# Kernel optimization log

Measured on AMD Instinct MI355X. Metric: run time of the kernel, lower is better.

The kernel has to match this reference:

```python
import jax, jax.numpy as jnp
import numpy as np
from jax import lax

B_, N_, DIM, HID, DST, NT, IR, DTR, HH, WW = 16, 4096, 192, 384, 16, 17, 128, 24, 64, 64


def _selective_scan(u, delta, A, Bs, Cs, D, delta_bias):
    # u, delta: (B, Din, L); A: (Din, N); Bs, Cs: (B, N, L); D, delta_bias: (Din,)
    delta = jax.nn.softplus(delta + delta_bias[None, :, None])
    dT = jnp.moveaxis(delta, 2, 0)   # (L, B, Din)
    uT = jnp.moveaxis(u, 2, 0)       # (L, B, Din)
    BT = jnp.moveaxis(Bs, 2, 0)      # (L, B, N)
    CT = jnp.moveaxis(Cs, 2, 0)      # (L, B, N)
    Bsz, Din, L = u.shape
    Nst = A.shape[1]
    h0 = jnp.zeros((Bsz, Din, Nst), u.dtype)

    def step(h, inp):
        d_l, u_l, b_l, c_l = inp
        da = jnp.exp(d_l[:, :, None] * A[None])              # (B, Din, N)
        h = da * h + (d_l * u_l)[:, :, None] * b_l[:, None, :]
        y = jnp.einsum('bdn,bn->bd', h, c_l)
        return h, y

    _, ys = lax.scan(step, h0, (dT, uT, BT, CT))
    y = jnp.moveaxis(ys, 0, 2)                               # (B, Din, L)
    return y + u * D[None, :, None]


def _assm_forward(x, token_weight, gumbel_noise, embB, route_w1, route_b1, route_w2,
                  route_b2, inproj_w, inproj_b, cpe_w, cpe_b, x_proj_w, dt_w, dt_b,
                  A_logs, Ds, norm_g, norm_b, outproj_w, outproj_b, H, W, gather_type):
    B, n, C = x.shape
    hidden = inproj_w.shape[0]
    dst = token_weight.shape[1]
    dtr = dt_w.shape[1]

    # routing + gumbel-softmax (hard, straight-through)
    full_emb = embB @ token_weight                           # (NT, d_state)
    hmid = jax.nn.gelu(x @ route_w1.T + route_b1)
    logits = jax.nn.log_softmax(hmid @ route_w2.T + route_b2, axis=-1)
    y_soft = jax.nn.softmax(logits + gumbel_noise, axis=-1)
    idx = jnp.argmax(y_soft, axis=-1)                        # (B, n)
    y_hard = jax.nn.one_hot(idx, logits.shape[-1], dtype=y_soft.dtype)
    cls_policy = y_hard + y_soft - lax.stop_gradient(y_soft)
    prompt = cls_policy @ full_emb                           # (B, n, d_state)

    det = lax.stop_gradient(idx)
    # (gather_type 3/5 keypoint-group remap omitted: gather_type == 1 here)
    sort_idx = jnp.argsort(det, axis=-1)                     # (B, n)
    inv_idx = jnp.argsort(sort_idx, axis=-1)                 # index_reverse

    # in_proj (1x1 conv == pointwise linear) then depthwise CPE gate
    xi = x @ inproj_w.T + inproj_b                           # (B, n, hidden)
    xg = xi.reshape(B, H, W, hidden).transpose(0, 3, 1, 2)   # NCHW
    cpe = lax.conv_general_dilated(xg, cpe_w, (1, 1), 'SAME',
                                   feature_group_count=hidden,
                                   dimension_numbers=('NCHW', 'OIHW', 'NCHW'))
    cpe = cpe + cpe_b[None, :, None, None]
    xg = xg * jax.nn.sigmoid(cpe)
    xflat = xg.reshape(B, hidden, n).transpose(0, 2, 1)      # (B, n, hidden)

    sem_x = jnp.take_along_axis(xflat, sort_idx[:, :, None], axis=1)

    # Selective_Scan core
    xs = sem_x.transpose(0, 2, 1)                            # (B, Din, L)
    x_dbl = jnp.einsum('bdl,cd->bcl', xs, x_proj_w)          # (B, dtr+2N, L)
    dts, Bs, Cs = jnp.split(x_dbl, [dtr, dtr + dst], axis=1)
    dts = jnp.einsum('brl,dr->bdl', dts, dt_w)
    if gather_type != 0:
        Cs = Cs + prompt.transpose(0, 2, 1)
    A = -jnp.exp(A_logs)
    y = _selective_scan(xs, dts, A, Bs, Cs, Ds, dt_b)        # (B, Din, L)
    y = y.transpose(0, 2, 1)                                 # (B, L, hidden)

    mu = jnp.mean(y, axis=-1, keepdims=True)
    var = jnp.mean(jnp.square(y - mu), axis=-1, keepdims=True)
    yn = (y - mu) / jnp.sqrt(var + 1e-5) * norm_g + norm_b
    out = yn @ outproj_w.T + outproj_b                       # (B, n, dim)
    out = jnp.take_along_axis(out, inv_idx[:, :, None], axis=1)
    return out


def setup_inputs() -> dict:
    key = jax.random.key(0)
    ks = jax.random.split(key, 16)

    def rn(k, sh, s=0.02):
        return jax.random.normal(k, sh, dtype=jnp.float32) * s

    u = jax.random.uniform(ks[0], (B_, N_, NT), jnp.float32, 1e-6, 1.0 - 1e-6)
    gumbel = -jnp.log(-jnp.log(u))

    # faithful dt bias init (inverse-softplus of log-uniform dt)
    rng = np.random.default_rng(0)
    dt = np.exp(rng.uniform(size=HID) * (np.log(0.1) - np.log(0.001)) + np.log(0.001))
    dt = np.clip(dt, 1e-4, None)
    inv_dt = dt + np.log(-np.expm1(-dt))

    A_logs = jnp.log(jnp.tile(jnp.arange(1, DST + 1, dtype=jnp.float32), (HID, 1)))

    return {
        'x': jax.random.normal(ks[1], (B_, N_, DIM), jnp.float32),
        'token_weight': rn(ks[2], (IR, DST), 0.1),
        'gumbel_noise': gumbel,
        'embB': jax.random.uniform(ks[3], (NT, IR), jnp.float32, -1.0 / NT, 1.0 / NT),
        'route_w1': rn(ks[4], (DIM // 3, DIM)),
        'route_b1': jnp.zeros((DIM // 3,), jnp.float32),
        'route_w2': rn(ks[5], (NT, DIM // 3)),
        'route_b2': jnp.zeros((NT,), jnp.float32),
        'inproj_w': rn(ks[6], (HID, DIM)),
        'inproj_b': jnp.zeros((HID,), jnp.float32),
        'cpe_w': rn(ks[7], (HID, 1, 3, 3), 0.1),
        'cpe_b': jnp.zeros((HID,), jnp.float32),
        'x_proj_w': rn(ks[8], (DTR + 2 * DST, HID)),
        'dt_w': jax.random.uniform(ks[9], (HID, DTR), jnp.float32, -DTR ** -0.5, DTR ** -0.5),
        'dt_b': jnp.asarray(inv_dt, jnp.float32),
        'A_logs': A_logs,
        'Ds': jnp.ones((HID,), jnp.float32),
        'norm_g': jnp.ones((HID,), jnp.float32),
        'norm_b': jnp.zeros((HID,), jnp.float32),
        'outproj_w': rn(ks[10], (DIM, HID)),
        'outproj_b': jnp.zeros((DIM,), jnp.float32),
        'H': HH,
        'W': WW,
        'gather_type': 1,
    }


def reference(x, token_weight, gumbel_noise, embB, route_w1, route_b1, route_w2,
              route_b2, inproj_w, inproj_b, cpe_w, cpe_b, x_proj_w, dt_w, dt_b,
              A_logs, Ds, norm_g, norm_b, outproj_w, outproj_b, H, W, gather_type):
    return _assm_forward(x, token_weight, gumbel_noise, embB, route_w1, route_b1,
                         route_w2, route_b2, inproj_w, inproj_b, cpe_w, cpe_b,
                         x_proj_w, dt_w, dt_b, A_logs, Ds, norm_g, norm_b,
                         outproj_w, outproj_b, H, W, gather_type)
```

## Files before the change

### kernel.cpp

```cpp
#include <hip/hip_runtime.h>
#include <math.h>

#define NB 16
#define NL 4096
#define ND 192
#define NH 384
#define NS 16
#define NTK 17
#define NIR 128
#define NR 24
#define NHH 64
#define NWW 64
#define NCHUNKS 32
#define CHUNKLEN 128
#define NTOK (NB*NL)

typedef __attribute__((ext_vector_type(8))) short short8;
typedef __attribute__((ext_vector_type(4))) float floatx4;

__device__ __forceinline__ float gelu_tanh(float x){
  return 0.5f*x*(1.0f + tanhf(0.7978845608028654f*(x + 0.044715f*x*x*x)));
}
__device__ __forceinline__ float softplus_f(float x){
  return (x > 20.0f) ? x : log1pf(expf(x));
}
__device__ __forceinline__ short f2bf(float f){
  unsigned u = __float_as_uint(f);
  unsigned r = (u + 0x7fffu + ((u >> 16) & 1u)) >> 16;
  return (short)r;
}

union Pack8 { uint4 v; short s[8]; };

__global__ void k_cvtw(const float* __restrict__ inw, const float* __restrict__ ow,
                       const float* __restrict__ xpw, const float* __restrict__ dtw,
                       short* __restrict__ inwb, short* __restrict__ owb,
                       short* __restrict__ xpwb, short* __restrict__ dtwb,
                       const float* __restrict__ embB, const float* __restrict__ tw,
                       float* __restrict__ fe){
  int i = blockIdx.x*256 + threadIdx.x;
  int stride = gridDim.x*256;
  for (int p = i; p < NH*ND; p += stride) inwb[p] = f2bf(inw[p]);
  for (int p = i; p < ND*NH; p += stride) owb[p] = f2bf(ow[p]);
  for (int p = i; p < 56*NH; p += stride) xpwb[p] = f2bf(xpw[p]);
  for (int p = i; p < NH*32; p += stride){
    int r = p >> 5, c = p & 31;
    dtwb[p] = (c < NR) ? f2bf(dtw[r*NR + c]) : (short)0;
  }
  if (blockIdx.x == 0){
    for (int o = threadIdx.x; o < NTK*NS; o += 256){
      int t = o / NS, s = o % NS;
      float acc = 0.f;
      for (int k = 0; k < NIR; ++k) acc += embB[t*NIR+k]*tw[k*NS+s];
      fe[o] = acc;
    }
  }
}

template<int EPI>
__global__ __launch_bounds__(256) void k_gemm(const float* __restrict__ A, int lda,
    const float* __restrict__ W, int ldw, const float* __restrict__ bias,
    float* __restrict__ C, int ldc, int N, int K){
  __shared__ float As[16][68];
  __shared__ float Ws[16][68];
  int tid = threadIdx.x;
  int m0 = blockIdx.x*64, n0 = blockIdx.y*64;
  int tx = tid & 15, ty = tid >> 4;
  int srow = tid >> 2, skseg = (tid & 3)*4;
  float acc[4][4] = {};
  for (int k0 = 0; k0 < K; k0 += 16){
    {
      const float* ap = A + (size_t)(m0+srow)*lda + k0 + skseg;
      float4 v = *(const float4*)ap;
      As[skseg+0][srow]=v.x; As[skseg+1][srow]=v.y;
      As[skseg+2][srow]=v.z; As[skseg+3][srow]=v.w;
    }
    {
      float4 v = {0.f,0.f,0.f,0.f};
      if (n0 + srow < N) v = *(const float4*)(W + (size_t)(n0+srow)*ldw + k0 + skseg);
      Ws[skseg+0][srow]=v.x; Ws[skseg+1][srow]=v.y;
      Ws[skseg+2][srow]=v.z; Ws[skseg+3][srow]=v.w;
    }
    __syncthreads();
    #pragma unroll
    for (int kk = 0; kk < 16; ++kk){
      float4 av = *(const float4*)&As[kk][ty*4];
      float4 wv = *(const float4*)&Ws[kk][tx*4];
      acc[0][0] += av.x*wv.x; acc[0][1] += av.x*wv.y;
      acc[0][2] += av.x*wv.z; acc[0][3] += av.x*wv.w;
      acc[1][0] += av.y*wv.x; acc[1][1] += av.y*wv.y;
      acc[1][2] += av.y*wv.z; acc[1][3] += av.y*wv.w;
      acc[2][0] += av.z*wv.x; acc[2][1] += av.z*wv.y;
      acc[2][2] += av.z*wv.z; acc[2][3] += av.z*wv.w;
      acc[3][0] += av.w*wv.x; acc[3][1] += av.w*wv.y;
      acc[3][2] += av.w*wv.z; acc[3][3] += av.w*wv.w;
    }
    __syncthreads();
  }
  #pragma unroll
  for (int i = 0; i < 4; ++i){
    int m = m0 + ty*4 + i;
    #pragma unroll
    for (int j = 0; j < 4; ++j){
      int n = n0 + tx*4 + j;
      if (n < N){
        float v = acc[i][j] + (bias ? bias[n] : 0.f);
        if (EPI==1) v = gelu_tanh(v);
        C[(size_t)m*ldc + n] = v;
      }
    }
  }
}

template<int EPI, int AF32, int LNA>
__global__ __launch_bounds__(256) void k_mfma(const void* __restrict__ Aptr, int lda,
    const short* __restrict__ Wbf, int ldw, const float* __restrict__ bias,
    float* __restrict__ C, int ldc, int N, int K, const int* __restrict__ remap,
    const float* __restrict__ lnm, const float* __restrict__ lnr,
    const float* __restrict__ lng, const float* __restrict__ lnb){
  __shared__ short As[128*40];
  __shared__ short Bs[64*40];
  int tid = threadIdx.x;
  int m0 = blockIdx.x*128, n0 = blockIdx.y*64;
  int w = tid >> 6, lane = tid & 63;
  int lq = lane >> 4, lr = lane & 15;
  floatx4 acc[2][4];
  #pragma unroll
  for (int i = 0; i < 2; ++i)
    #pragma unroll
    for (int j = 0; j < 4; ++j) acc[i][j] = (floatx4){0.f,0.f,0.f,0.f};
  int ar = tid >> 1, aq = (tid & 1)*2;
  int br = tid >> 2, bq = tid & 3;
  float mr = 0.f, rr = 0.f;
  if (LNA){ mr = lnm[m0+ar]; rr = lnr[m0+ar]; }
  for (int k0 = 0; k0 < K; k0 += 32){
    Pack8 sa0, sa1;
    if (AF32){
      const float* ap = (const float*)Aptr + (size_t)(m0+ar)*lda + k0 + aq*8;
      float f[16];
      float4 f0 = *(const float4*)(ap);
      float4 f1 = *(const float4*)(ap+4);
      float4 f2 = *(const float4*)(ap+8);
      float4 f3 = *(const float4*)(ap+12);
      f[0]=f0.x; f[1]=f0.y; f[2]=f0.z; f[3]=f0.w;
      f[4]=f1.x; f[5]=f1.y; f[6]=f1.z; f[7]=f1.w;
      f[8]=f2.x; f[9]=f2.y; f[10]=f2.z; f[11]=f2.w;
      f[12]=f3.x; f[13]=f3.y; f[14]=f3.z; f[15]=f3.w;
      if (LNA){
        const float* gp = lng + k0 + aq*8;
        const float* bp = lnb + k0 + aq*8;
        #pragma unroll
        for (int j = 0; j < 16; ++j) f[j] = (f[j]-mr)*rr*gp[j] + bp[j];
      }
      #pragma unroll
      for (int j = 0; j < 8; ++j){ sa0.s[j] = f2bf(f[j]); sa1.s[j] = f2bf(f[8+j]); }
    } else {
      const short* ap = (const short*)Aptr + (size_t)(m0+ar)*lda + k0 + aq*8;
      sa0.v = *(const uint4*)ap;
      sa1.v = *(const uint4*)(ap + 8);
    }
    uint4 bv = {0u,0u,0u,0u};
    if (n0 + br < N) bv = *(const uint4*)(Wbf + (size_t)(n0+br)*ldw + k0 + bq*8);
    __syncthreads();
    *(uint4*)&As[ar*40 + aq*8]     = sa0.v;
    *(uint4*)&As[ar*40 + aq*8 + 8] = sa1.v;
    *(uint4*)&Bs[br*40 + bq*8]     = bv;
    __syncthreads();
    short8 a0 = *(const short8*)&As[(w*32      + lr)*40 + lq*8];
    short8 a1 = *(const short8*)&As[(w*32 + 16 + lr)*40 + lq*8];
    short8 b0 = *(const short8*)&Bs[(     lr)*40 + lq*8];
    short8 b1 = *(const short8*)&Bs[(16 + lr)*40 + lq*8];
    short8 b2 = *(const short8*)&Bs[(32 + lr)*40 + lq*8];
    short8 b3 = *(const short8*)&Bs[(48 + lr)*40 + lq*8];
    acc[0][0] = __builtin_amdgcn_mfma_f32_16x16x32_bf16(a0, b0, acc[0][0], 0,0,0);
    acc[0][1] = __builtin_amdgcn_mfma_f32_16x16x32_bf16(a0, b1, acc[0][1], 0,0,0);
    acc[0][2] = __builtin_amdgcn_mfma_f32_16x16x32_bf16(a0, b2, acc[0][2], 0,0,0);
    acc[0][3] = __builtin_amdgcn_mfma_f32_16x16x32_bf16(a0, b3, acc[0][3], 0,0,0);
    acc[1][0] = __builtin_amdgcn_mfma_f32_16x16x32_bf16(a1, b0, acc[1][0], 0,0,0);
    acc[1][1] = __builtin_amdgcn_mfma_f32_16x16x32_bf16(a1, b1, acc[1][1], 0,0,0);
    acc[1][2] = __builtin_amdgcn_mfma_f32_16x16x32_bf16(a1, b2, acc[1][2], 0,0,0);
    acc[1][3] = __builtin_amdgcn_mfma_f32_16x16x32_bf16(a1, b3, acc[1][3], 0,0,0);
  }
  #pragma unroll
  for (int mt = 0; mt < 2; ++mt){
    #pragma unroll
    for (int r = 0; r < 4; ++r){
      int m = m0 + w*32 + mt*16 + lq*4 + r;
      int orow = (EPI==3) ? remap[m] : m;
      #pragma unroll
      for (int nt = 0; nt < 4; ++nt){
        int n = n0 + nt*16 + lr;
        if (n < N){
          float v = acc[mt][nt][r] + (bias ? bias[n] : 0.f);
          if (EPI==2) v = softplus_f(v);
          C[(size_t)orow*ldc + n] = v;
        }
      }
    }
  }
}

__global__ __launch_bounds__(256) void k_xdbl(const float* __restrict__ us,
    const short* __restrict__ xpwb, const int* __restrict__ idx,
    const float* __restrict__ fe, const int* __restrict__ gt,
    float* __restrict__ Bsb, float* __restrict__ Csb, short* __restrict__ dtsb){
  __shared__ short As[128*40];
  __shared__ short Bs[64*40];
  int tid = threadIdx.x;
  int m0 = blockIdx.x*128;
  int w = tid >> 6, lane = tid & 63;
  int lq = lane >> 4, lr = lane & 15;
  floatx4 acc[2][4];
  #pragma unroll
  for (int i = 0; i < 2; ++i)
    #pragma unroll
    for (int j = 0; j < 4; ++j) acc[i][j] = (floatx4){0.f,0.f,0.f,0.f};
  int ar = tid >> 1, aq = (tid & 1)*2;
  int br = tid >> 2, bq = tid & 3;
  for (int k0 = 0; k0 < NH; k0 += 32){
    Pack8 sa0, sa1;
    {
      const float* ap = us + (size_t)(m0+ar)*NH + k0 + aq*8;
      float f[16];
      float4 f0 = *(const float4*)(ap);
      float4 f1 = *(const float4*)(ap+4);
      float4 f2 = *(const float4*)(ap+8);
      float4 f3 = *(const float4*)(ap+12);
      f[0]=f0.x; f[1]=f0.y; f[2]=f0.z; f[3]=f0.w;
      f[4]=f1.x; f[5]=f1.y; f[6]=f1.z; f[7]=f1.w;
      f[8]=f2.x; f[9]=f2.y; f[10]=f2.z; f[11]=f2.w;
      f[12]=f3.x; f[13]=f3.y; f[14]=f3.z; f[15]=f3.w;
      #pragma unroll
      for (int j = 0; j < 8; ++j){ sa0.s[j] = f2bf(f[j]); sa1.s[j] = f2bf(f[8+j]); }
    }
    uint4 bv = {0u,0u,0u,0u};
    if (br < 56) bv = *(const uint4*)(xpwb + (size_t)br*NH + k0 + bq*8);
    __syncthreads();
    *(uint4*)&As[ar*40 + aq*8]     = sa0.v;
    *(uint4*)&As[ar*40 + aq*8 + 8] = sa1.v;
    *(uint4*)&Bs[br*40 + bq*8]     = bv;
    __syncthreads();
    short8 a0 = *(const short8*)&As[(w*32      + lr)*40 + lq*8];
    short8 a1 = *(const short8*)&As[(w*32 + 16 + lr)*40 + lq*8];
    short8 b0 = *(const short8*)&Bs[(     lr)*40 + lq*8];
    short8 b1 = *(const short8*)&Bs[(16 + lr)*40 + lq*8];
    short8 b2 = *(const short8*)&Bs[(32 + lr)*40 + lq*8];
    short8 b3 = *(const short8*)&Bs[(48 + lr)*40 + lq*8];
    acc[0][0] = __builtin_amdgcn_mfma_f32_16x16x32_bf16(a0, b0, acc[0][0], 0,0,0);
    acc[0][1] = __builtin_amdgcn_mfma_f32_16x16x32_bf16(a0, b1, acc[0][1], 0,0,0);
    acc[0][2] = __builtin_amdgcn_mfma_f32_16x16x32_bf16(a0, b2, acc[0][2], 0,0,0);
    acc[0][3] = __builtin_amdgcn_mfma_f32_16x16x32_bf16(a0, b3, acc[0][3], 0,0,0);
    acc[1][0] = __builtin_amdgcn_mfma_f32_16x16x32_bf16(a1, b0, acc[1][0], 0,0,0);
    acc[1][1] = __builtin_amdgcn_mfma_f32_16x16x32_bf16(a1, b1, acc[1][1], 0,0,0);
    acc[1][2] = __builtin_amdgcn_mfma_f32_16x16x32_bf16(a1, b2, acc[1][2], 0,0,0);
    acc[1][3] = __builtin_amdgcn_mfma_f32_16x16x32_bf16(a1, b3, acc[1][3], 0,0,0);
  }
  int gather = gt[0];
  #pragma unroll
  for (int mt = 0; mt < 2; ++mt){
    #pragma unroll
    for (int r = 0; r < 4; ++r){
      int m = m0 + w*32 + mt*16 + lq*4 + r;
      int id = idx[m];
      #pragma unroll
      for (int nt = 0; nt < 4; ++nt){
        int n = nt*16 + lr;
        float v = acc[mt][nt][r];
        if (n < 24){
          dtsb[(size_t)m*32 + n] = f2bf(v);
        } else if (n < 40){
          Bsb[(size_t)m*NS + (n-24)] = v;
          if (n < 32) dtsb[(size_t)m*32 + n] = 0;
        } else if (n < 56){
          float cv = v;
          if (gather != 0) cv += fe[id*NS + (n-40)];
          Csb[(size_t)m*NS + (n-40)] = cv;
        }
      }
    }
  }
}

__global__ __launch_bounds__(256) void k_argmax(const float* __restrict__ hmid,
    const float* __restrict__ w2, const float* __restrict__ b2,
    const float* __restrict__ gumbel, int* __restrict__ idx){
  int g = blockIdx.x*256 + threadIdx.x;
  float hm[64];
  const float4* hp = (const float4*)(hmid + (size_t)g*64);
  #pragma unroll
  for (int i = 0; i < 16; ++i){
    float4 v = hp[i];
    hm[i*4+0]=v.x; hm[i*4+1]=v.y; hm[i*4+2]=v.z; hm[i*4+3]=v.w;
  }
  float best = -INFINITY; int bi = 0;
  for (int c = 0; c < NTK; ++c){
    float s = b2[c] + gumbel[(size_t)g*NTK + c];
    #pragma unroll
    for (int j = 0; j < 64; ++j) s += hm[j]*w2[c*64+j];
    if (s > best){ best = s; bi = c; }
  }
  idx[g] = bi;
}

__global__ __launch_bounds__(256) void k_sort(const int* __restrict__ idx,
    int* __restrict__ rmap, int* __restrict__ inv){
  int b = blockIdx.x, t = threadIdx.x;
  __shared__ int hist[NTK][256];
  __shared__ int tot[NTK];
  __shared__ int keybase[NTK];
  int keys[16];
  const int* ip = idx + b*NL + t*16;
  #pragma unroll
  for (int i = 0; i < 16; ++i) keys[i] = ip[i];
  #pragma unroll
  for (int k = 0; k < NTK; ++k){
    int c = 0;
    #pragma unroll
    for (int i = 0; i < 16; ++i) c += (keys[i]==k) ? 1 : 0;
    hist[k][t] = c;
  }
  __syncthreads();
  if (t < NTK){
    int run = 0;
    for (int j = 0; j < 256; ++j){ int v = hist[t][j]; hist[t][j] = run; run += v; }
    tot[t] = run;
  }
  __syncthreads();
  if (t == 0){
    int base = 0;
    for (int k = 0; k < NTK; ++k){ keybase[k] = base; base += tot[k]; }
  }
  __syncthreads();
  #pragma unroll
  for (int i = 0; i < 16; ++i){
    int k = keys[i];
    int cb = 0;
    #pragma unroll
    for (int j = 0; j < 16; ++j) cb += (j < i && keys[j]==k) ? 1 : 0;
    int pos = keybase[k] + hist[k][t] + cb;
    rmap[b*NL + pos] = b*NL + t*16 + i;
    inv[b*NL + t*16 + i] = pos;
  }
}

__global__ __launch_bounds__(384) void k_cpe(const float* __restrict__ xi,
    const float* __restrict__ cw, const float* __restrict__ cb,
    const int* __restrict__ inv, float* __restrict__ us){
  int bl = blockIdx.x;
  int cg = bl & 3;
  int xt = (bl>>2) & 7;
  int yt = (bl>>5) & 7;
  int b  = bl >> 8;
  __shared__ float tile[10*10*96];
  int tx = threadIdx.x;
  int ty = threadIdx.y;
  int c0 = cg*96;
  int ch = c0 + tx;
  for (int yy = 0; yy < 10; ++yy){
    int gy = yt*8 + yy - 1;
    for (int xx = ty; xx < 10; xx += 4){
      int gx = xt*8 + xx - 1;
      float v = 0.f;
      if (gy >= 0 && gy < NHH && gx >= 0 && gx < NWW)
        v = xi[((size_t)(b*NL + gy*NWW + gx))*NH + ch];
      tile[(yy*10 + xx)*96 + tx] = v;
    }
  }
  float wreg[9];
  #pragma unroll
  for (int j = 0; j < 9; ++j) wreg[j] = cw[ch*9 + j];
  float bias = cb[ch];
  __syncthreads();
  for (int yy = ty; yy < 8; yy += 4){
    #pragma unroll
    for (int xx = 0; xx < 8; ++xx){
      float acc = bias;
      #pragma unroll
      for (int dy = 0; dy < 3; ++dy)
        #pragma unroll
        for (int dx = 0; dx < 3; ++dx)
          acc += tile[((yy+dy)*10 + (xx+dx))*96 + tx] * wreg[dy*3+dx];
      float center = tile[((yy+1)*10 + (xx+1))*96 + tx];
      float gate = 1.f/(1.f + expf(-acc));
      int l = (yt*8+yy)*NWW + xt*8+xx;
      int pos = inv[b*NL + l];
      us[((size_t)(b*NL + pos))*NH + ch] = center*gate;
    }
  }
}

__device__ __forceinline__ void decay16(bool pw, float dlt, const float* An, float* a){
  if (pw){
    float r  = __expf(dlt*An[0]);
    float r2 = r*r;
    float r3 = r2*r;
    float r4 = r2*r2;
    float r8 = r4*r4;
    float r12 = r8*r4;
    a[0]=r;     a[1]=r2;     a[2]=r3;     a[3]=r4;
    a[4]=r4*r;  a[5]=r4*r2;  a[6]=r4*r3;  a[7]=r8;
    a[8]=r8*r;  a[9]=r8*r2;  a[10]=r8*r3; a[11]=r12;
    a[12]=r12*r; a[13]=r12*r2; a[14]=r12*r3; a[15]=r8*r8;
  } else {
    #pragma unroll
    for (int n = 0; n < NS; ++n) a[n] = __expf(dlt*An[n]);
  }
}
__device__ __forceinline__ bool pwcheck(const float* An){
  bool pw = true;
  #pragma unroll
  for (int n = 1; n < NS; ++n)
    pw = pw && (fabsf(An[n] - (n+1)*An[0]) <= 1e-4f*fabsf(An[n]));
  return pw;
}

__global__ __launch_bounds__(384) void k_scan1(const float* __restrict__ delta,
    const float* __restrict__ us, const float* __restrict__ Bsb,
    const float* __restrict__ A_logs, float* __restrict__ sds, float* __restrict__ Boff){
  int bc = blockIdx.x;
  int c = bc & (NCHUNKS-1);
  int b = bc >> 5;
  int d = threadIdx.x;
  __shared__ float4 Bsh[CHUNKLEN*4];
  int base = b*NL + c*CHUNKLEN;
  {
    const float4* Bg = (const float4*)(Bsb + (size_t)base*NS);
    for (int p = d; p < CHUNKLEN*4; p += 384) Bsh[p] = Bg[p];
  }
  float An[NS];
  #pragma unroll
  for (int n = 0; n < NS; ++n) An[n] = -expf(A_logs[d*NS + n]);
  bool pw = pwcheck(An);
  float h[NS];
  #pragma unroll
  for (int n = 0; n < NS; ++n) h[n]=0.f;
  float sd = 0.f;
  __syncthreads();
  size_t gi = (size_t)base*NH + d;
  float dlt = delta[gi];
  float uv  = us[gi];
  #pragma unroll 2
  for (int s = 0; s < CHUNKLEN; ++s){
    float dltc = dlt, uvc = uv;
    if (s < CHUNKLEN-1){
      dlt = delta[gi + NH];
      uv  = us[gi + NH];
    }
    float du = dltc*uvc;
    sd += dltc;
    float a[NS];
    decay16(pw, dltc, An, a);
    float bb[NS];
    #pragma unroll
    for (int q = 0; q < 4; ++q) *(float4*)&bb[4*q] = Bsh[s*4 + q];
    #pragma unroll
    for (int n = 0; n < NS; ++n) h[n] = a[n]*h[n] + du*bb[n];
    gi += NH;
  }
  sds[(size_t)bc*NH + d] = sd;
  size_t o = ((size_t)bc*NH + d)*NS;
  *(float4*)(Boff + o)      = make_float4(h[0], h[1], h[2], h[3]);
  *(float4*)(Boff + o + 4)  = make_float4(h[4], h[5], h[6], h[7]);
  *(float4*)(Boff + o + 8)  = make_float4(h[8], h[9], h[10],h[11]);
  *(float4*)(Boff + o + 12) = make_float4(h[12],h[13],h[14],h[15]);
}

__global__ __launch_bounds__(256) void k_scan2(const float* __restrict__ A_logs,
    const float* __restrict__ sds, float* __restrict__ Boff){
  int i = blockIdx.x*256 + threadIdx.x;
  int dn = i % (NH*NS);
  int b = i / (NH*NS);
  float An = -expf(A_logs[dn]);
  int d = dn >> 4;
  float h = 0.f;
  for (int c = 0; c < NCHUNKS; ++c){
    int bc = b*NCHUNKS + c;
    float sd = sds[(size_t)bc*NH + d];
    float a = __expf(sd*An);
    size_t o = (size_t)bc*(NH*NS) + dn;
    float bo = Boff[o];
    Boff[o] = h;
    h = a*h + bo;
  }
}

__global__ __launch_bounds__(384) void k_scan3(const float* __restrict__ delta,
    const float* __restrict__ Bsb, const float* __restrict__ Csb,
    const float* __restrict__ A_logs, const float* __restrict__ Ds,
    const float* __restrict__ hinit, float* __restrict__ us,
    float* __restrict__ lnmean, float* __restrict__ lnrstd){
  int bc = blockIdx.x;
  int c = bc & (NCHUNKS-1);
  int b = bc >> 5;
  int d = threadIdx.x;
  __shared__ float4 Bsh[CHUNKLEN*4];
  __shared__ float4 Csh[CHUNKLEN*4];
  int base = b*NL + c*CHUNKLEN;
  {
    const float4* Bg = (const float4*)(Bsb + (size_t)base*NS);
    const float4* Cg = (const float4*)(Csb + (size_t)base*NS);
    for (int p = d; p < CHUNKLEN*4; p += 384){
      Bsh[p] = Bg[p];
      Csh[p] = Cg[p];
    }
  }
  float An[NS];
  #pragma unroll
  for (int n = 0; n < NS; ++n) An[n] = -expf(A_logs[d*NS + n]);
  bool pw = pwcheck(An);
  float h[NS];
  size_t ho = ((size_t)bc*NH + d)*NS;
  {
    float4 h0 = *(const float4*)(hinit + ho);
    float4 h1 = *(const float4*)(hinit + ho + 4);
    float4 h2 = *(const float4*)(hinit + ho + 8);
    float4 h3 = *(const float4*)(hinit + ho + 12);
    h[0]=h0.x; h[1]=h0.y; h[2]=h0.z; h[3]=h0.w;
    h[4]=h1.x; h[5]=h1.y; h[6]=h1.z; h[7]=h1.w;
    h[8]=h2.x; h[9]=h2.y; h[10]=h2.z; h[11]=h2.w;
    h[12]=h3.x; h[13]=h3.y; h[14]=h3.z; h[15]=h3.w;
  }
  float Dd = Ds[d];
  __syncthreads();
  size_t gi = (size_t)base*NH + d;
  float dlt = delta[gi];
  float uv  = us[gi];
  #pragma unroll 2
  for (int s = 0; s < CHUNKLEN; ++s){
    float dltc = dlt, uvc = uv;
    if (s < CHUNKLEN-1){
      dlt = delta[gi + NH];
      uv  = us[gi + NH];
    }
    float du = dltc*uvc;
    float a[NS];
    decay16(pw, dltc, An, a);
    float bb[NS], cc[NS];
    #pragma unroll
    for (int q = 0; q < 4; ++q){
      *(float4*)&bb[4*q] = Bsh[s*4 + q];
      *(float4*)&cc[4*q] = Csh[s*4 + q];
    }
    #pragma unroll
    for (int n = 0; n < NS; ++n) h[n] = a[n]*h[n] + du*bb[n];
    float ya = 0.f, yb = 0.f, yc = 0.f, yd = 0.f;
    #pragma unroll
    for (int q = 0; q < 4; ++q){
      ya += h[q]*cc[q];
      yb += h[4+q]*cc[4+q];
      yc += h[8+q]*cc[8+q];
      yd += h[12+q]*cc[12+q];
    }
    float y = (ya+yb)+(yc+yd);
    us[gi] = y + uvc*Dd;
    gi += NH;
  }
  __syncthreads();
  {
    int w = d >> 6, lane = d & 63;
    for (int t = w; t < CHUNKLEN; t += 6){
      int row = base + t;
      const float* rp = us + (size_t)row*NH;
      float v[6];
      #pragma unroll
      for (int i = 0; i < 6; ++i) v[i] = rp[i*64 + lane];
      float s = 0.f;
      #pragma unroll
      for (int i = 0; i < 6; ++i) s += v[i];
      #pragma unroll
      for (int off = 32; off > 0; off >>= 1) s += __shfl_xor(s, off);
      float mu = s * (1.f/NH);
      float vs = 0.f;
      #pragma unroll
      for (int i = 0; i < 6; ++i){ float dv = v[i]-mu; vs += dv*dv; }
      #pragma unroll
      for (int off = 32; off > 0; off >>= 1) vs += __shfl_xor(vs, off);
      float rs = rsqrtf(vs*(1.f/NH) + 1e-5f);
      if (lane == 0){ lnmean[row] = mu; lnrstd[row] = rs; }
    }
  }
}

extern "C" void kernel_launch(void* const* d_in, const int* in_sizes, int n_in,
                              void* d_out, int out_size, void* d_ws, size_t ws_size,
                              hipStream_t stream){
  const float* x      = (const float*)d_in[0];
  const float* tw     = (const float*)d_in[1];
  const float* gumbel = (const float*)d_in[2];
  const float* embB   = (const float*)d_in[3];
  const float* rw1    = (const float*)d_in[4];
  const float* rb1    = (const float*)d_in[5];
  const float* rw2    = (const float*)d_in[6];
  const float* rb2    = (const float*)d_in[7];
  const float* inw    = (const float*)d_in[8];
  const float* inb    = (const float*)d_in[9];
  const float* cw     = (const float*)d_in[10];
  const float* cb     = (const float*)d_in[11];
  const float* xpw    = (const float*)d_in[12];
  const float* dtw    = (const float*)d_in[13];
  const float* dtb    = (const float*)d_in[14];
  const float* A_logs = (const float*)d_in[15];
  const float* Ds     = (const float*)d_in[16];
  const float* ng     = (const float*)d_in[17];
  const float* nbv    = (const float*)d_in[18];
  const float* ow     = (const float*)d_in[19];
  const float* ob     = (const float*)d_in[20];
  const int*   gt     = (const int*)d_in[23];
  float* out = (float*)d_out;

  float* ws = (float*)d_ws;
  size_t o = 0;
  float* fe   = ws + o; o += 512;
  int* idx    = (int*)(ws + o); o += NTOK;
  int* rmap   = (int*)(ws + o); o += NTOK;
  int* inv    = (int*)(ws + o); o += NTOK;
  float* hmid = ws + o; o += (size_t)NTOK*64;
  float* xi   = ws + o; o += (size_t)NTOK*NH;
  float* us   = ws + o; o += (size_t)NTOK*NH;
  float* Bsb  = ws + o; o += (size_t)NTOK*NS;
  float* Csb  = ws + o; o += (size_t)NTOK*NS;
  float* sds  = ws + o; o += (size_t)NB*NCHUNKS*NH;
  float* Bof  = ws + o; o += (size_t)NB*NCHUNKS*NH*NS;
  short* inwb = (short*)(ws + o); o += (NH*ND)/2;
  short* owb  = (short*)(ws + o); o += (ND*NH)/2;
  short* xpwb = (short*)(ws + o); o += (56*NH)/2 + 32;
  short* dtwb = (short*)(ws + o); o += (NH*32)/2;
  float* delta = xi;
  short* dtsb = (short*)Bof;
  float* lnmean = (float*)idx;
  float* lnrstd = (float*)inv;

  k_cvtw<<<64,256,0,stream>>>(inw, ow, xpw, dtw, inwb, owb, xpwb, dtwb, embB, tw, fe);
  k_gemm<1><<<dim3(NTOK/64,1),256,0,stream>>>(x, ND, rw1, ND, rb1, hmid, 64, 64, ND);
  k_argmax<<<NTOK/256,256,0,stream>>>(hmid, rw2, rb2, gumbel, idx);
  k_sort<<<NB,256,0,stream>>>(idx, rmap, inv);
  k_mfma<0,1,0><<<dim3(NTOK/128,6),256,0,stream>>>(x, ND, inwb, ND, inb, xi, NH, NH, ND,
      nullptr, nullptr, nullptr, nullptr, nullptr);
  k_cpe<<<NB*64*4,dim3(96,4),0,stream>>>(xi, cw, cb, inv, us);
  k_xdbl<<<NTOK/128,256,0,stream>>>(us, xpwb, idx, fe, gt, Bsb, Csb, dtsb);
  k_mfma<2,0,0><<<dim3(NTOK/128,6),256,0,stream>>>(dtsb, 32, dtwb, 32, dtb, delta, NH, NH, 32,
      nullptr, nullptr, nullptr, nullptr, nullptr);
  k_scan1<<<NB*NCHUNKS,384,0,stream>>>(delta, us, Bsb, A_logs, sds, Bof);
  k_scan2<<<(NB*NH*NS)/256,256,0,stream>>>(A_logs, sds, Bof);
  k_scan3<<<NB*NCHUNKS,384,0,stream>>>(delta, Bsb, Csb, A_logs, Ds, Bof, us,
                                       lnmean, lnrstd);
  k_mfma<3,1,1><<<dim3(NTOK/128,3),256,0,stream>>>(us, NH, owb, NH, ob, out, ND, ND, NH,
      rmap, lnmean, lnrstd, ng, nbv);
}
```

Measured before the change: 689.8 us.

## Fuse routing GEMM with argmax and compute LayerNorm stats from shared-memory ring

Merges the routing MLP GEMM+GELU kernel with the argmax kernel, keeping the 64-wide hidden activations in shared memory instead of writing and rereading a global hmid buffer, and saving one launch. In the scan3 kernel, per-row outputs are also staged in a 32-row shared buffer so LayerNorm mean/rstd are computed every 32 steps from LDS rather than rereading us from global after the chunk. The cost is extra LDS use (about 48KB in scan3), which may lower occupancy, plus additional block barriers inside the sequential scan loop. Only 64 threads per block do the argmax, which limits parallelism in that phase.

Result: faster. 674.4 us (-2.2%).

```diff
diff --git a/kernel.cpp b/kernel.cpp
--- a/kernel.cpp
+++ b/kernel.cpp
@@ -57,27 +57,29 @@
   }
 }
 
-template<int EPI>
-__global__ __launch_bounds__(256) void k_gemm(const float* __restrict__ A, int lda,
-    const float* __restrict__ W, int ldw, const float* __restrict__ bias,
-    float* __restrict__ C, int ldc, int N, int K){
+__global__ __launch_bounds__(256) void k_route(const float* __restrict__ A,
+    const float* __restrict__ W, const float* __restrict__ b1,
+    const float* __restrict__ w2, const float* __restrict__ b2,
+    const float* __restrict__ gumbel, int* __restrict__ idx){
   __shared__ float As[16][68];
   __shared__ float Ws[16][68];
+  __shared__ float hm[64*65];
+  __shared__ float w2s[NTK*64];
   int tid = threadIdx.x;
-  int m0 = blockIdx.x*64, n0 = blockIdx.y*64;
+  int m0 = blockIdx.x*64;
   int tx = tid & 15, ty = tid >> 4;
   int srow = tid >> 2, skseg = (tid & 3)*4;
+  for (int p = tid; p < NTK*64; p += 256) w2s[p] = w2[p];
   float acc[4][4] = {};
-  for (int k0 = 0; k0 < K; k0 += 16){
+  for (int k0 = 0; k0 < ND; k0 += 16){
     {
-      const float* ap = A + (size_t)(m0+srow)*lda + k0 + skseg;
+      const float* ap = A + (size_t)(m0+srow)*ND + k0 + skseg;
       float4 v = *(const float4*)ap;
       As[skseg+0][srow]=v.x; As[skseg+1][srow]=v.y;
       As[skseg+2][srow]=v.z; As[skseg+3][srow]=v.w;
     }
     {
-      float4 v = {0.f,0.f,0.f,0.f};
-      if (n0 + srow < N) v = *(const float4*)(W + (size_t)(n0+srow)*ldw + k0 + skseg);
+      float4 v = *(const float4*)(W + (size_t)srow*ND + k0 + skseg);
       Ws[skseg+0][srow]=v.x; Ws[skseg+1][srow]=v.y;
       Ws[skseg+2][srow]=v.z; Ws[skseg+3][srow]=v.w;
     }
@@ -98,17 +100,22 @@
     __syncthreads();
   }
   #pragma unroll
-  for (int i = 0; i < 4; ++i){
-    int m = m0 + ty*4 + i;
-    #pragma unroll
-    for (int j = 0; j < 4; ++j){
-      int n = n0 + tx*4 + j;
-      if (n < N){
-        float v = acc[i][j] + (bias ? bias[n] : 0.f);
-        if (EPI==1) v = gelu_tanh(v);
-        C[(size_t)m*ldc + n] = v;
-      }
-    }
+  for (int i = 0; i < 4; ++i)
+    #pragma unroll
+    for (int j = 0; j < 4; ++j)
+      hm[(ty*4+i)*65 + tx*4+j] = gelu_tanh(acc[i][j] + b1[tx*4+j]);
+  __syncthreads();
+  if (tid < 64){
+    int g = m0 + tid;
+    const float* hr = &hm[tid*65];
+    float best = -INFINITY; int bi = 0;
+    for (int c = 0; c < NTK; ++c){
+      float s = b2[c] + gumbel[(size_t)g*NTK + c];
+      #pragma unroll
+      for (int j = 0; j < 64; ++j) s += hr[j]*w2s[c*64+j];
+      if (s > best){ best = s; bi = c; }
+    }
+    idx[g] = bi;
   }
 }
 
@@ -281,27 +288,6 @@
   }
 }
 
-__global__ __launch_bounds__(256) void k_argmax(const float* __restrict__ hmid,
-    const float* __restrict__ w2, const float* __restrict__ b2,
-    const float* __restrict__ gumbel, int* __restrict__ idx){
-  int g = blockIdx.x*256 + threadIdx.x;
-  float hm[64];
-  const float4* hp = (const float4*)(hmid + (size_t)g*64);
-  #pragma unroll
-  for (int i = 0; i < 16; ++i){
-    float4 v = hp[i];
-    hm[i*4+0]=v.x; hm[i*4+1]=v.y; hm[i*4+2]=v.z; hm[i*4+3]=v.w;
-  }
-  float best = -INFINITY; int bi = 0;
-  for (int c = 0; c < NTK; ++c){
-    float s = b2[c] + gumbel[(size_t)g*NTK + c];
-    #pragma unroll
-    for (int j = 0; j < 64; ++j) s += hm[j]*w2[c*64+j];
-    if (s > best){ best = s; bi = c; }
-  }
-  idx[g] = bi;
-}
-
 __global__ __launch_bounds__(256) void k_sort(const int* __restrict__ idx,
     int* __restrict__ rmap, int* __restrict__ inv){
   int b = blockIdx.x, t = threadIdx.x;
@@ -495,6 +481,7 @@
   int d = threadIdx.x;
   __shared__ float4 Bsh[CHUNKLEN*4];
   __shared__ float4 Csh[CHUNKLEN*4];
+  __shared__ float ybuf[32*384];
   int base = b*NL + c*CHUNKLEN;
   {
     const float4* Bg = (const float4*)(Bsb + (size_t)base*NS);
@@ -521,6 +508,7 @@
     h[12]=h3.x; h[13]=h3.y; h[14]=h3.z; h[15]=h3.w;
   }
   float Dd = Ds[d];
+  int wv = d >> 6, lane = d & 63;
   __syncthreads();
   size_t gi = (size_t)base*NH + d;
   float dlt = delta[gi];
@@ -551,32 +539,33 @@
       yc += h[8+q]*cc[8+q];
       yd += h[12+q]*cc[12+q];
     }
-    float y = (ya+yb)+(yc+yd);
-    us[gi] = y + uvc*Dd;
+    float y = ((ya+yb)+(yc+yd)) + uvc*Dd;
+    us[gi] = y;
+    ybuf[(s & 31)*384 + d] = y;
     gi += NH;
-  }
-  __syncthreads();
-  {
-    int w = d >> 6, lane = d & 63;
-    for (int t = w; t < CHUNKLEN; t += 6){
-      int row = base + t;
-      const float* rp = us + (size_t)row*NH;
-      float v[6];
-      #pragma unroll
-      for (int i = 0; i < 6; ++i) v[i] = rp[i*64 + lane];
-      float s = 0.f;
-      #pragma unroll
-      for (int i = 0; i < 6; ++i) s += v[i];
-      #pragma unroll
-      for (int off = 32; off > 0; off >>= 1) s += __shfl_xor(s, off);
-      float mu = s * (1.f/NH);
-      float vs = 0.f;
-      #pragma unroll
-      for (int i = 0; i < 6; ++i){ float dv = v[i]-mu; vs += dv*dv; }
-      #pragma unroll
-      for (int off = 32; off > 0; off >>= 1) vs += __shfl_xor(vs, off);
-      float rs = rsqrtf(vs*(1.f/NH) + 1e-5f);
-      if (lane == 0){ lnmean[row] = mu; lnrstd[row] = rs; }
+    if ((s & 31) == 31){
+      __syncthreads();
+      int ws0 = s - 31;
+      for (int t = wv; t < 32; t += 6){
+        const float* rp = &ybuf[t*384];
+        float v[6];
+        #pragma unroll
+        for (int i = 0; i < 6; ++i) v[i] = rp[i*64 + lane];
+        float sm = 0.f;
+        #pragma unroll
+        for (int i = 0; i < 6; ++i) sm += v[i];
+        #pragma unroll
+        for (int off = 32; off > 0; off >>= 1) sm += __shfl_xor(sm, off);
+        float mu = sm * (1.f/NH);
+        float vs = 0.f;
+        #pragma unroll
+        for (int i = 0; i < 6; ++i){ float dv = v[i]-mu; vs += dv*dv; }
+        #pragma unroll
+        for (int off = 32; off > 0; off >>= 1) vs += __shfl_xor(vs, off);
+        float rs = rsqrtf(vs*(1.f/NH) + 1e-5f);
+        if (lane == 0){ lnmean[base+ws0+t] = mu; lnrstd[base+ws0+t] = rs; }
+      }
+      __syncthreads();
     }
   }
 }
@@ -629,10 +618,10 @@
   short* dtsb = (short*)Bof;
   float* lnmean = (float*)idx;
   float* lnrstd = (float*)inv;
+  (void)hmid;
 
   k_cvtw<<<64,256,0,stream>>>(inw, ow, xpw, dtw, inwb, owb, xpwb, dtwb, embB, tw, fe);
-  k_gemm<1><<<dim3(NTOK/64,1),256,0,stream>>>(x, ND, rw1, ND, rb1, hmid, 64, 64, ND);
-  k_argmax<<<NTOK/256,256,0,stream>>>(hmid, rw2, rb2, gumbel, idx);
+  k_route<<<NTOK/64,256,0,stream>>>(x, rw1, rb1, rw2, rb2, gumbel, idx);
   k_sort<<<NB,256,0,stream>>>(idx, rmap, inv);
   k_mfma<0,1,0><<<dim3(NTOK/128,6),256,0,stream>>>(x, ND, inwb, ND, inb, xi, NH, NH, ND,
       nullptr, nullptr, nullptr, nullptr, nullptr);
```
